# Kernel tuning notes

Measured on AMD Instinct MI355X. Metric: run time of the kernel, lower is better.

Reference implementation:

```python
import jax, jax.numpy as jnp
import numpy as np
from jax import lax

NPOINT = 1024
NSAMPLE = 32
RADIUS = 0.2
EPS = 1e-5  # BatchNorm eps (torch default)


def farthest_point_sample(xyz, npoint):
    # xyz: [B, N, 3] -> [B, npoint] int32 indices. Deterministic start at index 0
    # (torch version uses a random start; math is otherwise identical).
    B, N, _ = xyz.shape

    def step(carry, _):
        distance, farthest = carry
        centroid = jnp.take_along_axis(xyz, farthest[:, None, None], axis=1)  # [B,1,3]
        d = jnp.sum((xyz - centroid) ** 2, axis=-1)                            # [B,N]
        distance = jnp.minimum(distance, d)
        return (distance, jnp.argmax(distance, axis=-1).astype(jnp.int32)), farthest

    init = (jnp.full((B, N), 1e10, xyz.dtype), jnp.zeros((B,), jnp.int32))
    _, cents = lax.scan(step, init, None, length=npoint)  # [npoint, B]
    return cents.T


def query_ball_point(radius, nsample, xyz, new_xyz):
    # xyz: [B,N,3], new_xyz: [B,S,3] -> [B,S,nsample] int32 indices
    B, N, _ = xyz.shape
    S = new_xyz.shape[1]
    sqr = jnp.sum((new_xyz[:, :, None, :] - xyz[:, None, :, :]) ** 2, axis=-1)  # [B,S,N]
    base = jnp.broadcast_to(jnp.arange(N, dtype=jnp.int32), (B, S, N))
    idx = jnp.where(sqr > radius * radius, N, base)
    idx = jnp.sort(idx, axis=-1)[:, :, :nsample]
    first = idx[:, :, :1]
    return jnp.where(idx == N, first, idx)


def index_points(points, idx):
    # points: [B,N,C], idx: [B,...] -> [B,...,C]
    return jax.vmap(lambda p, i: p[i])(points, idx)


def conv_bn_relu(x, w, b, g, beta):
    # 1x1 Conv2d == per-point linear; BatchNorm2d in training mode (batch stats,
    # biased variance) over all dims except channel.
    y = jnp.einsum('bskc,oc->bsko', x, w) + b          # [B,S,K,O]
    m = jnp.mean(y, axis=(0, 1, 2), keepdims=True)
    v = jnp.var(y, axis=(0, 1, 2), keepdims=True)
    return jax.nn.relu((y - m) / jnp.sqrt(v + EPS) * g + beta)


def setup_inputs() -> dict:
    key = jax.random.key(0)
    ks = jax.random.split(key, 8)
    B, N, D = 16, 4096, 64
    xyz = jax.random.uniform(ks[0], (B, N, 3), dtype=jnp.float32)
    points = jax.random.normal(ks[1], (B, N, D), dtype=jnp.float32)
    chans = [D + 3, 64, 64, 128]
    inp = {'xyz': xyz, 'points': points}
    for i in range(3):
        cin, cout = chans[i], chans[i + 1]
        inp[f'w{i}'] = jax.random.normal(ks[2 + i], (cout, cin), dtype=jnp.float32) * (1.0 / np.sqrt(cin))
        inp[f'b{i}'] = jnp.zeros((cout,), jnp.float32)
        inp[f'g{i}'] = jnp.ones((cout,), jnp.float32)
        inp[f'be{i}'] = jnp.zeros((cout,), jnp.float32)
    return inp


def reference(xyz, points, w0, b0, g0, be0, w1, b1, g1, be1, w2, b2, g2, be2):
    fps_idx = farthest_point_sample(xyz, NPOINT)            # [B,S]
    new_xyz = index_points(xyz, fps_idx)                    # [B,S,3]
    group_idx = query_ball_point(RADIUS, NSAMPLE, xyz, new_xyz)  # [B,S,K]
    grouped_xyz = index_points(xyz, group_idx) - new_xyz[:, :, None, :]  # [B,S,K,3]
    feats = jnp.concatenate([grouped_xyz, index_points(points, group_idx)], axis=-1)
    for (w, b, g, be) in ((w0, b0, g0, be0), (w1, b1, g1, be1), (w2, b2, g2, be2)):
        feats = conv_bn_relu(feats, w, b, g, be)
    new_points = jnp.max(feats, axis=2)                     # max over nsample -> [B,S,C_out]
    return new_xyz, new_points
```

## Files before the change

### kernel.cpp

```cpp
#include <hip/hip_runtime.h>
#include <hip/hip_bf16.h>
#include <cstdint>
#include <cstddef>

#define NPTS   4096
#define NPT    1024
#define NSAMP  32
#define NBATCH 16
#define MROWS  (NBATCH*NPT*NSAMP)
#define EPSV   1e-5f

typedef __attribute__((ext_vector_type(8))) short bfrag;
typedef __attribute__((ext_vector_type(4))) float f32x4;
typedef __attribute__((ext_vector_type(2))) float f32x2;

static __device__ __forceinline__ unsigned short f2bf(float f) {
  union { float f; unsigned u; } x; x.f = f;
  unsigned u = x.u;
  u += 0x7FFFu + ((u >> 16) & 1u);
  return (unsigned short)(u >> 16);
}
static __device__ __forceinline__ float bf2f(unsigned short h) {
  union { unsigned u; float f; } x; x.u = ((unsigned)h) << 16;
  return x.f;
}
static __device__ __forceinline__ unsigned cvt_pk_bf16(float lo, float hi) {
  unsigned r;
  asm("v_cvt_pk_bf16_f32 %0, %1, %2" : "=v"(r) : "v"(lo), "v"(hi));
  return r;
}

__global__ __launch_bounds__(256) void prep_kernel(
    const float* __restrict__ w0, const float* __restrict__ w1,
    const float* __restrict__ w2, unsigned short* __restrict__ wb0,
    unsigned short* __restrict__ wb1, unsigned short* __restrict__ wb2) {
  const int tid = threadIdx.x;
  for (int i = tid; i < 64 * 96; i += 256) {
    const int o = i / 96, c = i % 96;
    float v;
    if (c < 64)      v = w0[o * 67 + 3 + c];
    else if (c < 67) v = w0[o * 67 + (c - 64)];
    else             v = 0.f;
    wb0[i] = f2bf(v);
  }
  for (int i = tid; i < 64 * 64; i += 256) wb1[i] = f2bf(w1[i]);
  for (int i = tid; i < 128 * 64; i += 256) wb2[i] = f2bf(w2[i]);
}

#define FPS_T 256
#define PPT   (NPTS / FPS_T)

template <int CTRL>
static __device__ __forceinline__ float dpp_max_step(float v) {
  int t = __builtin_amdgcn_update_dpp(0, __float_as_int(v), CTRL, 0xF, 0xF, true);
  return fmaxf(v, __int_as_float(t));
}

__global__ __launch_bounds__(FPS_T) void fps_kernel(
    const float* __restrict__ xyz, float* __restrict__ out_newxyz) {
  __shared__ __align__(16) float xs[NPTS];
  __shared__ __align__(16) float ys[NPTS];
  __shared__ __align__(16) float zs[NPTS];
  __shared__ __align__(16) float olds[NPT * 3];
  __shared__ __align__(16) uint2 sl[2][4];

  const int b = blockIdx.x;
  const int tid = threadIdx.x;
  const int wave = tid >> 6;
  const float* base = xyz + (size_t)b * NPTS * 3;
  for (int i = tid; i < NPTS; i += FPS_T) {
    xs[i] = base[3 * i + 0];
    ys[i] = base[3 * i + 1];
    zs[i] = base[3 * i + 2];
  }
  __syncthreads();

  const int p0 = tid * PPT;
  f32x2 px2[8], py2[8], pz2[8], d2[8];
  #pragma unroll
  for (int p = 0; p < 8; ++p) {
    px2[p] = f32x2{xs[p0 + 2 * p], xs[p0 + 2 * p + 1]};
    py2[p] = f32x2{ys[p0 + 2 * p], ys[p0 + 2 * p + 1]};
    pz2[p] = f32x2{zs[p0 + 2 * p], zs[p0 + 2 * p + 1]};
    d2[p] = f32x2{1e10f, 1e10f};
  }

  int cur = 0;
  for (int it = 0; it < NPT; ++it) {
    const float cx = xs[cur], cy = ys[cur], cz = zs[cur];
    if (tid == 0) {
      olds[3 * it + 0] = cx;
      olds[3 * it + 1] = cy;
      olds[3 * it + 2] = cz;
    }
    if (it == NPT - 1) break;

    float bestv = -1.f; int besti = p0;
    {
      #pragma clang fp contract(off)
      const f32x2 c2x = {cx, cx}, c2y = {cy, cy}, c2z = {cz, cz};
      #pragma unroll
      for (int p = 0; p < 8; ++p) {
        const f32x2 dx = px2[p] - c2x;
        const f32x2 dy = py2[p] - c2y;
        const f32x2 dz = pz2[p] - c2z;
        const f32x2 s = (dx * dx + dy * dy) + dz * dz;
        f32x2 nd = d2[p];
        nd.x = fminf(nd.x, s.x);
        nd.y = fminf(nd.y, s.y);
        d2[p] = nd;
        const float pmax = fmaxf(nd.x, nd.y);
        const bool yg = nd.y > nd.x;
        const int pidx = p0 + 2 * p + (yg ? 1 : 0);
        const bool g = pmax > bestv;
        bestv = g ? pmax : bestv;
        besti = g ? pidx : besti;
      }
    }

    float m = bestv;
    m = dpp_max_step<0x111>(m);
    m = dpp_max_step<0x112>(m);
    m = dpp_max_step<0x114>(m);
    m = dpp_max_step<0x118>(m);
    m = dpp_max_step<0x142>(m);
    m = dpp_max_step<0x143>(m);
    const float wmax =
        __int_as_float(__builtin_amdgcn_readlane(__float_as_int(m), 63));

    const unsigned long long mask = __ballot(bestv == wmax);
    const int wl = __ffsll((long long)mask) - 1;
    const int widx = __builtin_amdgcn_readlane(besti, wl);

    const int buf = it & 1;
    if ((tid & 63) == 0)
      sl[buf][wave] = make_uint2(__float_as_uint(wmax), (unsigned)widx);
    __syncthreads();

    const uint4* p4 = (const uint4*)&sl[buf][0];
    const uint4 q0 = p4[0], q1 = p4[1];
    float bv; int bi;
    {
      bv = __uint_as_float(q0.x); bi = (int)q0.y;
      const float v1 = __uint_as_float(q0.z);
      if (v1 > bv) { bv = v1; bi = (int)q0.w; }
      const float v2 = __uint_as_float(q1.x);
      if (v2 > bv) { bv = v2; bi = (int)q1.y; }
      const float v3 = __uint_as_float(q1.z);
      if (v3 > bv) { bv = v3; bi = (int)q1.w; }
    }
    cur = bi;
  }

  __syncthreads();
  float* outb = out_newxyz + (size_t)b * NPT * 3;
  for (int i = tid; i < NPT * 3 / 4; i += FPS_T)
    *(float4*)&outb[4 * i] = *(const float4*)&olds[4 * i];
}

__global__ __launch_bounds__(256) void ballquery_kernel(
    const float* __restrict__ xyz, const float* __restrict__ newxyz,
    int* __restrict__ gidx) {
  const int gw = (int)((blockIdx.x * 256 + threadIdx.x) >> 6);
  const int lane = threadIdx.x & 63;
  const int b = gw >> 10, s = gw & 1023;
  const float* base = xyz + (size_t)b * NPTS * 3;
  const float* c = newxyz + (size_t)(b * NPT + s) * 3;
  const float cx = c[0], cy = c[1], cz = c[2];
  const float R2 = (float)(0.2 * 0.2);
  int* g = gidx + (size_t)(b * NPT + s) * NSAMP;

  int count = 0;
  int first = -1;
  for (int ch = 0; ch < NPTS / 64; ++ch) {
    const int i = ch * 64 + lane;
    const float dx = __fsub_rn(base[3 * i + 0], cx);
    const float dy = __fsub_rn(base[3 * i + 1], cy);
    const float dz = __fsub_rn(base[3 * i + 2], cz);
    const float d = __fadd_rn(__fadd_rn(__fmul_rn(dx, dx), __fmul_rn(dy, dy)),
                              __fmul_rn(dz, dz));
    const bool pred = !(d > R2);
    const unsigned long long mask = __ballot(pred);
    if (mask) {
      if (count == 0) first = ch * 64 + (__ffsll((long long)mask) - 1);
      const int rank = __popcll(mask & ((1ull << lane) - 1ull));
      const int pos = count + rank;
      if (pred && pos < NSAMP) g[pos] = i;
      count += (int)__popcll(mask);
      if (count >= NSAMP) break;
    }
  }
  if (first < 0) first = 0;
  for (int j = count + lane; j < NSAMP; j += 64) g[j] = first;
}

__global__ __launch_bounds__(256) void mm1_mfma_kernel(
    const float* __restrict__ xyz, const float* __restrict__ points,
    const float* __restrict__ newxyz, const int* __restrict__ gidx,
    const unsigned short* __restrict__ Wb, unsigned short* __restrict__ Y,
    float* __restrict__ psum, float* __restrict__ psq) {
  constexpr int KP = 104;
  __shared__ __align__(16) unsigned short As[64 * KP];
  __shared__ __align__(16) unsigned short ly[64 * 64];
  __shared__ float ssum[64], ssq[64];
  const int tid = threadIdx.x, bid = blockIdx.x;
  const size_t r0 = (size_t)bid * 64;

  {
    const int row = tid >> 2, q = tid & 3;
    const int gs = bid * 2 + (row >> 5);
    const int b = gs >> 10;
    const int k = row & 31;
    const int gpt = gidx[(size_t)gs * NSAMP + k];
    const float* pf = points + ((size_t)b * NPTS + gpt) * 64 + 16 * q;
    float f[16];
    #pragma unroll
    for (int i = 0; i < 4; ++i)
      *(float4*)&f[4 * i] = *(const float4*)&pf[4 * i];
    uint4 u0, u1;
    u0.x = cvt_pk_bf16(f[0], f[1]);   u0.y = cvt_pk_bf16(f[2], f[3]);
    u0.z = cvt_pk_bf16(f[4], f[5]);   u0.w = cvt_pk_bf16(f[6], f[7]);
    u1.x = cvt_pk_bf16(f[8], f[9]);   u1.y = cvt_pk_bf16(f[10], f[11]);
    u1.z = cvt_pk_bf16(f[12], f[13]); u1.w = cvt_pk_bf16(f[14], f[15]);
    uint4* dst = (uint4*)&As[row * KP + 16 * q];
    dst[0] = u0; dst[1] = u1;
    if (q == 0) {
      const float* px = xyz + ((size_t)b * NPTS + gpt) * 3;
      const float* pc = newxyz + (size_t)gs * 3;
      const float rx = px[0] - pc[0];
      const float ry = px[1] - pc[1];
      const float rz = px[2] - pc[2];
      uint4* d2 = (uint4*)&As[row * KP + 64];
      d2[0] = uint4{cvt_pk_bf16(rx, ry), cvt_pk_bf16(rz, 0.f), 0u, 0u};
      d2[1] = uint4{0u, 0u, 0u, 0u};
      d2[2] = uint4{0u, 0u, 0u, 0u};
      d2[3] = uint4{0u, 0u, 0u, 0u};
    }
  }
  if (tid < 64) { ssum[tid] = 0.f; ssq[tid] = 0.f; }
  __syncthreads();

  const int wave = tid >> 6, lane = tid & 63;
  const int l15 = lane & 15, kq = lane >> 4;
  const unsigned short* abase = &As[(wave * 16 + l15) * KP + kq * 8];
  const bfrag a0 = *(const bfrag*)abase;
  const bfrag a1 = *(const bfrag*)(abase + 32);
  const bfrag a2 = *(const bfrag*)(abase + 64);

  #pragma unroll
  for (int nt = 0; nt < 4; ++nt) {
    const unsigned short* wsrc = Wb + (size_t)(nt * 16 + l15) * 96 + kq * 8;
    const bfrag b0 = *(const bfrag*)wsrc;
    const bfrag b1 = *(const bfrag*)(wsrc + 32);
    const bfrag b2 = *(const bfrag*)(wsrc + 64);
    f32x4 acc = {0.f, 0.f, 0.f, 0.f};
    acc = __builtin_amdgcn_mfma_f32_16x16x32_bf16(a0, b0, acc, 0, 0, 0);
    acc = __builtin_amdgcn_mfma_f32_16x16x32_bf16(a1, b1, acc, 0, 0, 0);
    acc = __builtin_amdgcn_mfma_f32_16x16x32_bf16(a2, b2, acc, 0, 0, 0);

    float s = acc[0] + acc[1] + acc[2] + acc[3];
    float q = acc[0]*acc[0] + acc[1]*acc[1] + acc[2]*acc[2] + acc[3]*acc[3];
    s += __shfl_xor(s, 16); q += __shfl_xor(q, 16);
    s += __shfl_xor(s, 32); q += __shfl_xor(q, 32);
    if (kq == 0) {
      atomicAdd(&ssum[nt * 16 + l15], s);
      atomicAdd(&ssq [nt * 16 + l15], q);
    }
    const unsigned p01 = cvt_pk_bf16(acc[0], acc[1]);
    const unsigned p23 = cvt_pk_bf16(acc[2], acc[3]);
    const int colo = nt * 16 + l15;
    const int rbase = wave * 16 + kq * 4;
    ly[(rbase + 0) * 64 + colo] = (unsigned short)(p01 & 0xffffu);
    ly[(rbase + 1) * 64 + colo] = (unsigned short)(p01 >> 16);
    ly[(rbase + 2) * 64 + colo] = (unsigned short)(p23 & 0xffffu);
    ly[(rbase + 3) * 64 + colo] = (unsigned short)(p23 >> 16);
  }
  __syncthreads();
  {
    const uint4* lsrc = (const uint4*)ly;
    uint4* gdst = (uint4*)(Y + r0 * 64);
    #pragma unroll
    for (int i = tid; i < 64 * 64 * 2 / 16; i += 256) gdst[i] = lsrc[i];
  }
  if (tid < 64) {
    psum[(size_t)bid * 64 + tid] = ssum[tid];
    psq [(size_t)bid * 64 + tid] = ssq [tid];
  }
}

static __device__ __forceinline__ bfrag affine_relu_frag(
    const unsigned short* __restrict__ src, const float* __restrict__ st,
    int c0) {
  union { bfrag f; unsigned u[4]; } r;
  const uint4 raw = *(const uint4*)src;
  const unsigned w[4] = {raw.x, raw.y, raw.z, raw.w};
  #pragma unroll
  for (int p = 0; p < 4; ++p) {
    const int c = c0 + 2 * p;
    float lo = bf2f((unsigned short)(w[p] & 0xffffu));
    float hi = bf2f((unsigned short)(w[p] >> 16));
    lo = fmaxf(fmaf(lo, st[2 * c + 0], st[2 * c + 1]), 0.f);
    hi = fmaxf(fmaf(hi, st[2 * c + 2], st[2 * c + 3]), 0.f);
    r.u[p] = cvt_pk_bf16(lo, hi);
  }
  return r.f;
}

template <int COUT, int WAVES>
__global__ __launch_bounds__(WAVES * 64) void mm_mfma_kernel(
    const unsigned short* __restrict__ Xin, const unsigned short* __restrict__ Wb,
    const float* __restrict__ stin, unsigned short* __restrict__ Y,
    float* __restrict__ psum, float* __restrict__ psq) {
  constexpr int NT = COUT / 16;
  constexpr int ROWS = WAVES * 16;
  __shared__ float ssum[COUT], ssq[COUT];
  __shared__ __align__(16) unsigned short ly[ROWS * COUT];
  const int tid = threadIdx.x, bid = blockIdx.x;
  const int wave = tid >> 6, lane = tid & 63;
  const int l15 = lane & 15, kq = lane >> 4;
  const size_t r0 = (size_t)bid * ROWS;
  if (tid < COUT) { ssum[tid] = 0.f; ssq[tid] = 0.f; }

  const int arow = wave * 16 + l15;
  const unsigned short* asrc = Xin + (r0 + arow) * 64 + kq * 8;
  const bfrag a0 = affine_relu_frag(asrc, stin, kq * 8);
  const bfrag a1 = affine_relu_frag(asrc + 32, stin, 32 + kq * 8);
  __syncthreads();

  #pragma unroll
  for (int nt = 0; nt < NT; ++nt) {
    const unsigned short* wsrc = Wb + (size_t)(nt * 16 + l15) * 64 + kq * 8;
    const bfrag b0 = *(const bfrag*)wsrc;
    const bfrag b1 = *(const bfrag*)(wsrc + 32);
    f32x4 acc = {0.f, 0.f, 0.f, 0.f};
    acc = __builtin_amdgcn_mfma_f32_16x16x32_bf16(a0, b0, acc, 0, 0, 0);
    acc = __builtin_amdgcn_mfma_f32_16x16x32_bf16(a1, b1, acc, 0, 0, 0);

    float s = acc[0] + acc[1] + acc[2] + acc[3];
    float q = acc[0]*acc[0] + acc[1]*acc[1] + acc[2]*acc[2] + acc[3]*acc[3];
    s += __shfl_xor(s, 16); q += __shfl_xor(q, 16);
    s += __shfl_xor(s, 32); q += __shfl_xor(q, 32);
    if (kq == 0) {
      atomicAdd(&ssum[nt * 16 + l15], s);
      atomicAdd(&ssq [nt * 16 + l15], q);
    }
    const unsigned p01 = cvt_pk_bf16(acc[0], acc[1]);
    const unsigned p23 = cvt_pk_bf16(acc[2], acc[3]);
    const int colo = nt * 16 + l15;
    const int rbase = wave * 16 + kq * 4;
    ly[(rbase + 0) * COUT + colo] = (unsigned short)(p01 & 0xffffu);
    ly[(rbase + 1) * COUT + colo] = (unsigned short)(p01 >> 16);
    ly[(rbase + 2) * COUT + colo] = (unsigned short)(p23 & 0xffffu);
    ly[(rbase + 3) * COUT + colo] = (unsigned short)(p23 >> 16);
  }
  __syncthreads();
  {
    const uint4* lsrc = (const uint4*)ly;
    uint4* gdst = (uint4*)(Y + r0 * COUT);
    #pragma unroll
    for (int i = tid; i < ROWS * COUT * 2 / 16; i += WAVES * 64) gdst[i] = lsrc[i];
  }
  if (tid < COUT) {
    psum[(size_t)bid * COUT + tid] = ssum[tid];
    psq [(size_t)bid * COUT + tid] = ssq [tid];
  }
}

__global__ __launch_bounds__(512) void mm3_pool_kernel(
    const unsigned short* __restrict__ Xin, const unsigned short* __restrict__ Wb,
    const float* __restrict__ stin, float* __restrict__ pooled,
    float* __restrict__ psum, float* __restrict__ psq) {
  constexpr int COUT = 128, NT = 8;
  __shared__ float ssum[COUT], ssq[COUT];
  __shared__ float pm[8][COUT];
  const int tid = threadIdx.x, bid = blockIdx.x;
  const int wave = tid >> 6, lane = tid & 63;
  const int l15 = lane & 15, kq = lane >> 4;
  const size_t r0 = (size_t)bid * 128;
  if (tid < COUT) { ssum[tid] = 0.f; ssq[tid] = 0.f; }

  const int arow = wave * 16 + l15;
  const unsigned short* asrc = Xin + (r0 + arow) * 64 + kq * 8;
  const bfrag a0 = affine_relu_frag(asrc, stin, kq * 8);
  const bfrag a1 = affine_relu_frag(asrc + 32, stin, 32 + kq * 8);
  __syncthreads();

  #pragma unroll
  for (int nt = 0; nt < NT; ++nt) {
    const unsigned short* wsrc = Wb + (size_t)(nt * 16 + l15) * 64 + kq * 8;
    const bfrag b0 = *(const bfrag*)wsrc;
    const bfrag b1 = *(const bfrag*)(wsrc + 32);
    f32x4 acc = {0.f, 0.f, 0.f, 0.f};
    acc = __builtin_amdgcn_mfma_f32_16x16x32_bf16(a0, b0, acc, 0, 0, 0);
    acc = __builtin_amdgcn_mfma_f32_16x16x32_bf16(a1, b1, acc, 0, 0, 0);

    float s = acc[0] + acc[1] + acc[2] + acc[3];
    float q = acc[0]*acc[0] + acc[1]*acc[1] + acc[2]*acc[2] + acc[3]*acc[3];
    s += __shfl_xor(s, 16); q += __shfl_xor(q, 16);
    s += __shfl_xor(s, 32); q += __shfl_xor(q, 32);
    float mx = fmaxf(fmaxf(acc[0], acc[1]), fmaxf(acc[2], acc[3]));
    mx = fmaxf(mx, __shfl_xor(mx, 16));
    mx = fmaxf(mx, __shfl_xor(mx, 32));
    if (kq == 0) {
      atomicAdd(&ssum[nt * 16 + l15], s);
      atomicAdd(&ssq [nt * 16 + l15], q);
      pm[wave][nt * 16 + l15] = mx;
    }
  }
  __syncthreads();
  {
    const int g = tid >> 7, col = tid & 127;
    const float v = fmaxf(pm[2 * g][col], pm[2 * g + 1][col]);
    pooled[(r0 >> 5) * COUT + g * COUT + col] = v;
  }
  if (tid < COUT) {
    psum[(size_t)bid * COUT + tid] = ssum[tid];
    psq [(size_t)bid * COUT + tid] = ssq [tid];
  }
}

__global__ __launch_bounds__(256) void finalize_kernel(
    const float* __restrict__ psum, const float* __restrict__ psq,
    const float* __restrict__ gam, const float* __restrict__ bet,
    float* __restrict__ st, int C, int nb) {
  const int c = blockIdx.x, tid = threadIdx.x;
  float s = 0.f, q = 0.f;
  for (int i = tid; i < nb; i += 256) {
    s += psum[(size_t)i * C + c];
    q += psq [(size_t)i * C + c];
  }
  #pragma unroll
  for (int off = 32; off > 0; off >>= 1) {
    s += __shfl_down(s, off);
    q += __shfl_down(q, off);
  }
  __shared__ float as_[4], aq_[4];
  if ((tid & 63) == 0) { as_[tid >> 6] = s; aq_[tid >> 6] = q; }
  __syncthreads();
  if (tid == 0) {
    s = as_[0] + as_[1] + as_[2] + as_[3];
    q = aq_[0] + aq_[1] + aq_[2] + aq_[3];
    const float invM = 1.f / (float)MROWS;
    const float mean = s * invM;
    const float var = q * invM - mean * mean;
    const float inv = 1.f / sqrtf(var + EPSV);
    const float sc = gam[c] * inv;
    st[2 * c + 0] = sc;
    st[2 * c + 1] = bet[c] - mean * sc;
  }
}

__global__ __launch_bounds__(256) void bn_relu_kernel(
    const float* __restrict__ pooled, const float* __restrict__ st,
    float* __restrict__ out) {
  __shared__ float s_st[256];
  const int tid = threadIdx.x;
  s_st[tid] = st[tid];
  __syncthreads();
  const int n4 = NBATCH * NPT * 128 / 4;
  for (int i = blockIdx.x * 256 + tid; i < n4; i += gridDim.x * 256) {
    float4 v = ((const float4*)pooled)[i];
    const int c0 = (i * 4) & 127;
    v.x = fmaxf(fmaf(v.x, s_st[2 * c0 + 0], s_st[2 * c0 + 1]), 0.f);
    v.y = fmaxf(fmaf(v.y, s_st[2 * c0 + 2], s_st[2 * c0 + 3]), 0.f);
    v.z = fmaxf(fmaf(v.z, s_st[2 * c0 + 4], s_st[2 * c0 + 5]), 0.f);
    v.w = fmaxf(fmaf(v.w, s_st[2 * c0 + 6], s_st[2 * c0 + 7]), 0.f);
    ((float4*)out)[i] = v;
  }
}

extern "C" void kernel_launch(void* const* d_in, const int* in_sizes, int n_in,
                              void* d_out, int out_size, void* d_ws, size_t ws_size,
                              hipStream_t stream) {
  (void)in_sizes; (void)n_in; (void)out_size; (void)ws_size;
  const float* xyz    = (const float*)d_in[0];
  const float* points = (const float*)d_in[1];
  const float* w0 = (const float*)d_in[2];
  const float* g0 = (const float*)d_in[4];
  const float* be0 = (const float*)d_in[5];
  const float* w1 = (const float*)d_in[6];
  const float* g1 = (const float*)d_in[8];
  const float* be1 = (const float*)d_in[9];
  const float* w2 = (const float*)d_in[10];
  const float* g2 = (const float*)d_in[12];
  const float* be2 = (const float*)d_in[13];

  float* out = (float*)d_out;
  float* newxyz = out;
  float* newpts = out + (size_t)NBATCH * NPT * 3;

  char* ws = (char*)d_ws;
  unsigned short* Y1 = (unsigned short*)ws;
  float* P3 = (float*)ws;
  unsigned short* Y2 = (unsigned short*)(ws + 134217728);
  int*   gidx = (int*)  (ws + 201326592);
  float* psum = (float*)(ws + 203423744);
  float* psq  = (float*)(ws + 205520896);
  float* st   = (float*)(ws + 207618048);
  float* st1 = st, *st2 = st + 256, *st3 = st + 512;
  unsigned short* wb0 = (unsigned short*)(ws + 207621120);
  unsigned short* wb1 = (unsigned short*)(ws + 207621120 + 12288);
  unsigned short* wb2 = (unsigned short*)(ws + 207621120 + 12288 + 8192);

  prep_kernel<<<1, 256, 0, stream>>>(w0, w1, w2, wb0, wb1, wb2);
  fps_kernel<<<NBATCH, FPS_T, 0, stream>>>(xyz, newxyz);
  ballquery_kernel<<<(NBATCH * NPT) / 4, 256, 0, stream>>>(xyz, newxyz, gidx);
  mm1_mfma_kernel<<<MROWS / 64, 256, 0, stream>>>(xyz, points, newxyz, gidx, wb0, Y1, psum, psq);
  finalize_kernel<<<64, 256, 0, stream>>>(psum, psq, g0, be0, st1, 64, MROWS / 64);
  mm_mfma_kernel<64, 4><<<MROWS / 64, 256, 0, stream>>>(Y1, wb1, st1, Y2, psum, psq);
  finalize_kernel<<<64, 256, 0, stream>>>(psum, psq, g1, be1, st2, 64, MROWS / 64);
  mm3_pool_kernel<<<MROWS / 128, 512, 0, stream>>>(Y2, wb2, st2, P3, psum, psq);
  finalize_kernel<<<128, 256, 0, stream>>>(psum, psq, g2, be2, st3, 128, MROWS / 128);
  bn_relu_kernel<<<2048, 256, 0, stream>>>(P3, st3, newpts);
}
```

Measured before the change: 863.4 us.

## Fuse FPS, ball query and first matmul into one persistent producer-consumer kernel

Merges the farthest-point-sampling, ball-query and first MFMA layer into a single persistent kernel. Sixteen blocks run FPS and publish centroids in chunks of 128 through global progress counters. The remaining blocks pull tiles from an atomic work counter, spin-wait until their centroids are ready, then run the ball query into shared memory and the first matmul. The point is to overlap the long serial FPS with downstream work and to drop the global group-index buffer. The cost is spin-waiting on flags, a dependence on all blocks being co-resident, and an FPS loop that is no longer vectorised as float2.

```diff
diff --git a/kernel.cpp b/kernel.cpp
--- a/kernel.cpp
+++ b/kernel.cpp
@@ -8,11 +8,11 @@
 #define NSAMP  32
 #define NBATCH 16
 #define MROWS  (NBATCH*NPT*NSAMP)
+#define NTILES (MROWS / 64)
 #define EPSV   1e-5f
 
 typedef __attribute__((ext_vector_type(8))) short bfrag;
 typedef __attribute__((ext_vector_type(4))) float f32x4;
-typedef __attribute__((ext_vector_type(2))) float f32x2;
 
 static __device__ __forceinline__ unsigned short f2bf(float f) {
   union { float f; unsigned u; } x; x.f = f;
@@ -33,8 +33,10 @@
 __global__ __launch_bounds__(256) void prep_kernel(
     const float* __restrict__ w0, const float* __restrict__ w1,
     const float* __restrict__ w2, unsigned short* __restrict__ wb0,
-    unsigned short* __restrict__ wb1, unsigned short* __restrict__ wb2) {
+    unsigned short* __restrict__ wb1, unsigned short* __restrict__ wb2,
+    int* __restrict__ flags) {
   const int tid = threadIdx.x;
+  for (int i = tid; i < 260; i += 256) flags[i] = 0;
   for (int i = tid; i < 64 * 96; i += 256) {
     const int o = i / 96, c = i % 96;
     float v;
@@ -49,6 +51,7 @@
 
 #define FPS_T 256
 #define PPT   (NPTS / FPS_T)
+#define CHUNK 128
 
 template <int CTRL>
 static __device__ __forceinline__ float dpp_max_step(float v) {
@@ -56,235 +59,255 @@
   return fmaxf(v, __int_as_float(t));
 }
 
-__global__ __launch_bounds__(FPS_T) void fps_kernel(
-    const float* __restrict__ xyz, float* __restrict__ out_newxyz) {
+__global__ __launch_bounds__(256) void k1_kernel(
+    const float* __restrict__ xyz, const float* __restrict__ points,
+    const unsigned short* __restrict__ Wb, float* __restrict__ newxyz,
+    unsigned short* __restrict__ Y1, float* __restrict__ psum,
+    float* __restrict__ psq, int* __restrict__ flags) {
   __shared__ __align__(16) float xs[NPTS];
   __shared__ __align__(16) float ys[NPTS];
   __shared__ __align__(16) float zs[NPTS];
   __shared__ __align__(16) float olds[NPT * 3];
   __shared__ __align__(16) uint2 sl[2][4];
-
-  const int b = blockIdx.x;
-  const int tid = threadIdx.x;
-  const int wave = tid >> 6;
-  const float* base = xyz + (size_t)b * NPTS * 3;
-  for (int i = tid; i < NPTS; i += FPS_T) {
-    xs[i] = base[3 * i + 0];
-    ys[i] = base[3 * i + 1];
-    zs[i] = base[3 * i + 2];
-  }
-  __syncthreads();
-
-  const int p0 = tid * PPT;
-  f32x2 px2[8], py2[8], pz2[8], d2[8];
-  #pragma unroll
-  for (int p = 0; p < 8; ++p) {
-    px2[p] = f32x2{xs[p0 + 2 * p], xs[p0 + 2 * p + 1]};
-    py2[p] = f32x2{ys[p0 + 2 * p], ys[p0 + 2 * p + 1]};
-    pz2[p] = f32x2{zs[p0 + 2 * p], zs[p0 + 2 * p + 1]};
-    d2[p] = f32x2{1e10f, 1e10f};
-  }
-
-  int cur = 0;
-  for (int it = 0; it < NPT; ++it) {
-    const float cx = xs[cur], cy = ys[cur], cz = zs[cur];
-    if (tid == 0) {
-      olds[3 * it + 0] = cx;
-      olds[3 * it + 1] = cy;
-      olds[3 * it + 2] = cz;
-    }
-    if (it == NPT - 1) break;
-
-    float bestv = -1.f; int besti = p0;
-    {
-      #pragma clang fp contract(off)
-      const f32x2 c2x = {cx, cx}, c2y = {cy, cy}, c2z = {cz, cz};
-      #pragma unroll
-      for (int p = 0; p < 8; ++p) {
-        const f32x2 dx = px2[p] - c2x;
-        const f32x2 dy = py2[p] - c2y;
-        const f32x2 dz = pz2[p] - c2z;
-        const f32x2 s = (dx * dx + dy * dy) + dz * dz;
-        f32x2 nd = d2[p];
-        nd.x = fminf(nd.x, s.x);
-        nd.y = fminf(nd.y, s.y);
-        d2[p] = nd;
-        const float pmax = fmaxf(nd.x, nd.y);
-        const bool yg = nd.y > nd.x;
-        const int pidx = p0 + 2 * p + (yg ? 1 : 0);
-        const bool g = pmax > bestv;
-        bestv = g ? pmax : bestv;
-        besti = g ? pidx : besti;
-      }
-    }
-
-    float m = bestv;
-    m = dpp_max_step<0x111>(m);
-    m = dpp_max_step<0x112>(m);
-    m = dpp_max_step<0x114>(m);
-    m = dpp_max_step<0x118>(m);
-    m = dpp_max_step<0x142>(m);
-    m = dpp_max_step<0x143>(m);
-    const float wmax =
-        __int_as_float(__builtin_amdgcn_readlane(__float_as_int(m), 63));
-
-    const unsigned long long mask = __ballot(bestv == wmax);
-    const int wl = __ffsll((long long)mask) - 1;
-    const int widx = __builtin_amdgcn_readlane(besti, wl);
-
-    const int buf = it & 1;
-    if ((tid & 63) == 0)
-      sl[buf][wave] = make_uint2(__float_as_uint(wmax), (unsigned)widx);
-    __syncthreads();
-
-    const uint4* p4 = (const uint4*)&sl[buf][0];
-    const uint4 q0 = p4[0], q1 = p4[1];
-    float bv; int bi;
-    {
-      bv = __uint_as_float(q0.x); bi = (int)q0.y;
-      const float v1 = __uint_as_float(q0.z);
-      if (v1 > bv) { bv = v1; bi = (int)q0.w; }
-      const float v2 = __uint_as_float(q1.x);
-      if (v2 > bv) { bv = v2; bi = (int)q1.y; }
-      const float v3 = __uint_as_float(q1.z);
-      if (v3 > bv) { bv = v3; bi = (int)q1.w; }
-    }
-    cur = bi;
-  }
-
-  __syncthreads();
-  float* outb = out_newxyz + (size_t)b * NPT * 3;
-  for (int i = tid; i < NPT * 3 / 4; i += FPS_T)
-    *(float4*)&outb[4 * i] = *(const float4*)&olds[4 * i];
-}
-
-__global__ __launch_bounds__(256) void ballquery_kernel(
-    const float* __restrict__ xyz, const float* __restrict__ newxyz,
-    int* __restrict__ gidx) {
-  const int gw = (int)((blockIdx.x * 256 + threadIdx.x) >> 6);
-  const int lane = threadIdx.x & 63;
-  const int b = gw >> 10, s = gw & 1023;
-  const float* base = xyz + (size_t)b * NPTS * 3;
-  const float* c = newxyz + (size_t)(b * NPT + s) * 3;
-  const float cx = c[0], cy = c[1], cz = c[2];
-  const float R2 = (float)(0.2 * 0.2);
-  int* g = gidx + (size_t)(b * NPT + s) * NSAMP;
-
-  int count = 0;
-  int first = -1;
-  for (int ch = 0; ch < NPTS / 64; ++ch) {
-    const int i = ch * 64 + lane;
-    const float dx = __fsub_rn(base[3 * i + 0], cx);
-    const float dy = __fsub_rn(base[3 * i + 1], cy);
-    const float dz = __fsub_rn(base[3 * i + 2], cz);
-    const float d = __fadd_rn(__fadd_rn(__fmul_rn(dx, dx), __fmul_rn(dy, dy)),
-                              __fmul_rn(dz, dz));
-    const bool pred = !(d > R2);
-    const unsigned long long mask = __ballot(pred);
-    if (mask) {
-      if (count == 0) first = ch * 64 + (__ffsll((long long)mask) - 1);
-      const int rank = __popcll(mask & ((1ull << lane) - 1ull));
-      const int pos = count + rank;
-      if (pred && pos < NSAMP) g[pos] = i;
-      count += (int)__popcll(mask);
-      if (count >= NSAMP) break;
-    }
-  }
-  if (first < 0) first = 0;
-  for (int j = count + lane; j < NSAMP; j += 64) g[j] = first;
-}
-
-__global__ __launch_bounds__(256) void mm1_mfma_kernel(
-    const float* __restrict__ xyz, const float* __restrict__ points,
-    const float* __restrict__ newxyz, const int* __restrict__ gidx,
-    const unsigned short* __restrict__ Wb, unsigned short* __restrict__ Y,
-    float* __restrict__ psum, float* __restrict__ psq) {
   constexpr int KP = 104;
   __shared__ __align__(16) unsigned short As[64 * KP];
   __shared__ __align__(16) unsigned short ly[64 * 64];
   __shared__ float ssum[64], ssq[64];
-  const int tid = threadIdx.x, bid = blockIdx.x;
-  const size_t r0 = (size_t)bid * 64;
-
-  {
-    const int row = tid >> 2, q = tid & 3;
-    const int gs = bid * 2 + (row >> 5);
-    const int b = gs >> 10;
-    const int k = row & 31;
-    const int gpt = gidx[(size_t)gs * NSAMP + k];
-    const float* pf = points + ((size_t)b * NPTS + gpt) * 64 + 16 * q;
-    float f[16];
+  __shared__ int   gidxL[64];
+  __shared__ float cents[8];
+  __shared__ int   s_tile;
+
+  const int tid = threadIdx.x;
+  int* progress = flags;
+  int* counter  = flags + 256;
+
+  if (blockIdx.x < NBATCH) {
+    const int b = blockIdx.x;
+    const int wave = tid >> 6;
+    const float* base = xyz + (size_t)b * NPTS * 3;
+    float* outb = newxyz + (size_t)b * NPT * 3;
+    int* prog = &progress[b * 16];
+    for (int i = tid; i < NPTS; i += FPS_T) {
+      xs[i] = base[3 * i + 0];
+      ys[i] = base[3 * i + 1];
+      zs[i] = base[3 * i + 2];
+    }
+    __syncthreads();
+
+    const int p0 = tid * PPT;
+    float px[PPT], py[PPT], pz[PPT], dist[PPT];
     #pragma unroll
-    for (int i = 0; i < 4; ++i)
-      *(float4*)&f[4 * i] = *(const float4*)&pf[4 * i];
-    uint4 u0, u1;
-    u0.x = cvt_pk_bf16(f[0], f[1]);   u0.y = cvt_pk_bf16(f[2], f[3]);
-    u0.z = cvt_pk_bf16(f[4], f[5]);   u0.w = cvt_pk_bf16(f[6], f[7]);
-    u1.x = cvt_pk_bf16(f[8], f[9]);   u1.y = cvt_pk_bf16(f[10], f[11]);
-    u1.z = cvt_pk_bf16(f[12], f[13]); u1.w = cvt_pk_bf16(f[14], f[15]);
-    uint4* dst = (uint4*)&As[row * KP + 16 * q];
-    dst[0] = u0; dst[1] = u1;
-    if (q == 0) {
-      const float* px = xyz + ((size_t)b * NPTS + gpt) * 3;
-      const float* pc = newxyz + (size_t)gs * 3;
-      const float rx = px[0] - pc[0];
-      const float ry = px[1] - pc[1];
-      const float rz = px[2] - pc[2];
-      uint4* d2 = (uint4*)&As[row * KP + 64];
-      d2[0] = uint4{cvt_pk_bf16(rx, ry), cvt_pk_bf16(rz, 0.f), 0u, 0u};
-      d2[1] = uint4{0u, 0u, 0u, 0u};
-      d2[2] = uint4{0u, 0u, 0u, 0u};
-      d2[3] = uint4{0u, 0u, 0u, 0u};
-    }
-  }
-  if (tid < 64) { ssum[tid] = 0.f; ssq[tid] = 0.f; }
-  __syncthreads();
+    for (int i = 0; i < PPT; i += 4) {
+      *(float4*)&px[i] = *(const float4*)&xs[p0 + i];
+      *(float4*)&py[i] = *(const float4*)&ys[p0 + i];
+      *(float4*)&pz[i] = *(const float4*)&zs[p0 + i];
+    }
+    #pragma unroll
+    for (int i = 0; i < PPT; ++i) dist[i] = 1e10f;
+
+    int cur = 0;
+    for (int it = 0; it < NPT; ++it) {
+      const float cx = xs[cur], cy = ys[cur], cz = zs[cur];
+      if (tid == 0) {
+        olds[3 * it + 0] = cx;
+        olds[3 * it + 1] = cy;
+        olds[3 * it + 2] = cz;
+      }
+      if ((it & (CHUNK - 1)) == CHUNK - 1) {
+        __syncthreads();
+        const int cs = it - (CHUNK - 1);
+        if (tid < 96)
+          *(float4*)&outb[cs * 3 + tid * 4] =
+              *(const float4*)&olds[cs * 3 + tid * 4];
+        __threadfence();
+        __syncthreads();
+        if (tid == 0) atomicAdd(prog, CHUNK);
+      }
+      if (it == NPT - 1) break;
+
+      float bestv = -1.f; int besti = p0;
+      #pragma unroll
+      for (int i = 0; i < PPT; ++i) {
+        const float dx = __fsub_rn(px[i], cx);
+        const float dy = __fsub_rn(py[i], cy);
+        const float dz = __fsub_rn(pz[i], cz);
+        const float d = __fadd_rn(__fadd_rn(__fmul_rn(dx, dx), __fmul_rn(dy, dy)),
+                                  __fmul_rn(dz, dz));
+        const float nd = fminf(dist[i], d);
+        dist[i] = nd;
+        const bool g = nd > bestv;
+        bestv = g ? nd : bestv;
+        besti = g ? (p0 + i) : besti;
+      }
+
+      float m = bestv;
+      m = dpp_max_step<0x111>(m);
+      m = dpp_max_step<0x112>(m);
+      m = dpp_max_step<0x114>(m);
+      m = dpp_max_step<0x118>(m);
+      m = dpp_max_step<0x142>(m);
+      m = dpp_max_step<0x143>(m);
+      const float wmax =
+          __int_as_float(__builtin_amdgcn_readlane(__float_as_int(m), 63));
+
+      const unsigned long long mask = __ballot(bestv == wmax);
+      const int wl = __ffsll((long long)mask) - 1;
+      const int widx = __builtin_amdgcn_readlane(besti, wl);
+
+      const int buf = it & 1;
+      if ((tid & 63) == 0)
+        sl[buf][wave] = make_uint2(__float_as_uint(wmax), (unsigned)widx);
+      __syncthreads();
+
+      const uint4* p4 = (const uint4*)&sl[buf][0];
+      const uint4 q0 = p4[0], q1 = p4[1];
+      float bv; int bi;
+      {
+        bv = __uint_as_float(q0.x); bi = (int)q0.y;
+        const float v1 = __uint_as_float(q0.z);
+        if (v1 > bv) { bv = v1; bi = (int)q0.w; }
+        const float v2 = __uint_as_float(q1.x);
+        if (v2 > bv) { bv = v2; bi = (int)q1.y; }
+        const float v3 = __uint_as_float(q1.z);
+        if (v3 > bv) { bv = v3; bi = (int)q1.w; }
+      }
+      cur = bi;
+    }
+    return;
+  }
 
   const int wave = tid >> 6, lane = tid & 63;
-  const int l15 = lane & 15, kq = lane >> 4;
-  const unsigned short* abase = &As[(wave * 16 + l15) * KP + kq * 8];
-  const bfrag a0 = *(const bfrag*)abase;
-  const bfrag a1 = *(const bfrag*)(abase + 32);
-  const bfrag a2 = *(const bfrag*)(abase + 64);
-
-  #pragma unroll
-  for (int nt = 0; nt < 4; ++nt) {
-    const unsigned short* wsrc = Wb + (size_t)(nt * 16 + l15) * 96 + kq * 8;
-    const bfrag b0 = *(const bfrag*)wsrc;
-    const bfrag b1 = *(const bfrag*)(wsrc + 32);
-    const bfrag b2 = *(const bfrag*)(wsrc + 64);
-    f32x4 acc = {0.f, 0.f, 0.f, 0.f};
-    acc = __builtin_amdgcn_mfma_f32_16x16x32_bf16(a0, b0, acc, 0, 0, 0);
-    acc = __builtin_amdgcn_mfma_f32_16x16x32_bf16(a1, b1, acc, 0, 0, 0);
-    acc = __builtin_amdgcn_mfma_f32_16x16x32_bf16(a2, b2, acc, 0, 0, 0);
-
-    float s = acc[0] + acc[1] + acc[2] + acc[3];
-    float q = acc[0]*acc[0] + acc[1]*acc[1] + acc[2]*acc[2] + acc[3]*acc[3];
-    s += __shfl_xor(s, 16); q += __shfl_xor(q, 16);
-    s += __shfl_xor(s, 32); q += __shfl_xor(q, 32);
-    if (kq == 0) {
-      atomicAdd(&ssum[nt * 16 + l15], s);
-      atomicAdd(&ssq [nt * 16 + l15], q);
-    }
-    const unsigned p01 = cvt_pk_bf16(acc[0], acc[1]);
-    const unsigned p23 = cvt_pk_bf16(acc[2], acc[3]);
-    const int colo = nt * 16 + l15;
-    const int rbase = wave * 16 + kq * 4;
-    ly[(rbase + 0) * 64 + colo] = (unsigned short)(p01 & 0xffffu);
-    ly[(rbase + 1) * 64 + colo] = (unsigned short)(p01 >> 16);
-    ly[(rbase + 2) * 64 + colo] = (unsigned short)(p23 & 0xffffu);
-    ly[(rbase + 3) * 64 + colo] = (unsigned short)(p23 >> 16);
-  }
-  __syncthreads();
-  {
-    const uint4* lsrc = (const uint4*)ly;
-    uint4* gdst = (uint4*)(Y + r0 * 64);
+  for (;;) {
+    if (tid == 0) {
+      const int t0 = atomicAdd(counter, 1);
+      s_tile = t0;
+      if (t0 < NTILES) {
+        const int b = t0 & 15, s0 = (t0 >> 4) * 2;
+        while (__hip_atomic_load(&progress[b * 16], __ATOMIC_ACQUIRE,
+                                 __HIP_MEMORY_SCOPE_AGENT) < s0 + 2)
+          __builtin_amdgcn_s_sleep(2);
+      }
+    }
+    __syncthreads();
+    const int t = s_tile;
+    if (t >= NTILES) break;
+    const int b = t & 15, s0 = (t >> 4) * 2;
+
+    if (wave < 2) {
+      const int gs = b * NPT + s0 + wave;
+      const float* base = xyz + (size_t)b * NPTS * 3;
+      const float* c = newxyz + (size_t)gs * 3;
+      const float cx = c[0], cy = c[1], cz = c[2];
+      if (lane == 0) {
+        cents[wave * 4 + 0] = cx;
+        cents[wave * 4 + 1] = cy;
+        cents[wave * 4 + 2] = cz;
+      }
+      const float R2 = (float)(0.2 * 0.2);
+      int* g = &gidxL[wave * 32];
+      int count = 0;
+      int first = -1;
+      for (int ch = 0; ch < NPTS / 64; ++ch) {
+        const int i = ch * 64 + lane;
+        const float dx = __fsub_rn(base[3 * i + 0], cx);
+        const float dy = __fsub_rn(base[3 * i + 1], cy);
+        const float dz = __fsub_rn(base[3 * i + 2], cz);
+        const float d = __fadd_rn(
+            __fadd_rn(__fmul_rn(dx, dx), __fmul_rn(dy, dy)), __fmul_rn(dz, dz));
+        const bool pred = !(d > R2);
+        const unsigned long long mask = __ballot(pred);
+        if (mask) {
+          if (count == 0) first = ch * 64 + (__ffsll((long long)mask) - 1);
+          const int rank = __popcll(mask & ((1ull << lane) - 1ull));
+          const int pos = count + rank;
+          if (pred && pos < NSAMP) g[pos] = i;
+          count += (int)__popcll(mask);
+          if (count >= NSAMP) break;
+        }
+      }
+      if (first < 0) first = 0;
+      for (int j = count + lane; j < NSAMP; j += 64) g[j] = first;
+    }
+    if (tid < 64) { ssum[tid] = 0.f; ssq[tid] = 0.f; }
+    __syncthreads();
+
+    {
+      const int row = tid >> 2, q = tid & 3;
+      const int gpt = gidxL[row];
+      const float* pf = points + ((size_t)b * NPTS + gpt) * 64 + 16 * q;
+      float f[16];
+      #pragma unroll
+      for (int i = 0; i < 4; ++i)
+        *(float4*)&f[4 * i] = *(const float4*)&pf[4 * i];
+      uint4 u0, u1;
+      u0.x = cvt_pk_bf16(f[0], f[1]);   u0.y = cvt_pk_bf16(f[2], f[3]);
+      u0.z = cvt_pk_bf16(f[4], f[5]);   u0.w = cvt_pk_bf16(f[6], f[7]);
+      u1.x = cvt_pk_bf16(f[8], f[9]);   u1.y = cvt_pk_bf16(f[10], f[11]);
+      u1.z = cvt_pk_bf16(f[12], f[13]); u1.w = cvt_pk_bf16(f[14], f[15]);
+      uint4* dst = (uint4*)&As[row * KP + 16 * q];
+      dst[0] = u0; dst[1] = u1;
+      if (q == 0) {
+        const float* px = xyz + ((size_t)b * NPTS + gpt) * 3;
+        const float* pc = &cents[(row >> 5) * 4];
+        const float rx = px[0] - pc[0];
+        const float ry = px[1] - pc[1];
+        const float rz = px[2] - pc[2];
+        uint4* d2 = (uint4*)&As[row * KP + 64];
+        d2[0] = uint4{cvt_pk_bf16(rx, ry), cvt_pk_bf16(rz, 0.f), 0u, 0u};
+        d2[1] = uint4{0u, 0u, 0u, 0u};
+        d2[2] = uint4{0u, 0u, 0u, 0u};
+        d2[3] = uint4{0u, 0u, 0u, 0u};
+      }
+    }
+    __syncthreads();
+
+    const int l15 = lane & 15, kq = lane >> 4;
+    const unsigned short* abase = &As[(wave * 16 + l15) * KP + kq * 8];
+    const bfrag a0 = *(const bfrag*)abase;
+    const bfrag a1 = *(const bfrag*)(abase + 32);
+    const bfrag a2 = *(const bfrag*)(abase + 64);
+
     #pragma unroll
-    for (int i = tid; i < 64 * 64 * 2 / 16; i += 256) gdst[i] = lsrc[i];
-  }
-  if (tid < 64) {
-    psum[(size_t)bid * 64 + tid] = ssum[tid];
-    psq [(size_t)bid * 64 + tid] = ssq [tid];
+    for (int nt = 0; nt < 4; ++nt) {
+      const unsigned short* wsrc = Wb + (size_t)(nt * 16 + l15) * 96 + kq * 8;
+      const bfrag b0 = *(const bfrag*)wsrc;
+      const bfrag b1 = *(const bfrag*)(wsrc + 32);
+      const bfrag b2 = *(const bfrag*)(wsrc + 64);
+      f32x4 acc = {0.f, 0.f, 0.f, 0.f};
+      acc = __builtin_amdgcn_mfma_f32_16x16x32_bf16(a0, b0, acc, 0, 0, 0);
+      acc = __builtin_amdgcn_mfma_f32_16x16x32_bf16(a1, b1, acc, 0, 0, 0);
+      acc = __builtin_amdgcn_mfma_f32_16x16x32_bf16(a2, b2, acc, 0, 0, 0);
+
+      float s = acc[0] + acc[1] + acc[2] + acc[3];
+      float q = acc[0]*acc[0] + acc[1]*acc[1] + acc[2]*acc[2] + acc[3]*acc[3];
+      s += __shfl_xor(s, 16); q += __shfl_xor(q, 16);
+      s += __shfl_xor(s, 32); q += __shfl_xor(q, 32);
+      if (kq == 0) {
+        atomicAdd(&ssum[nt * 16 + l15], s);
+        atomicAdd(&ssq [nt * 16 + l15], q);
+      }
+      const unsigned p01 = cvt_pk_bf16(acc[0], acc[1]);
+      const unsigned p23 = cvt_pk_bf16(acc[2], acc[3]);
+      const int colo = nt * 16 + l15;
+      const int rbase = wave * 16 + kq * 4;
+      ly[(rbase + 0) * 64 + colo] = (unsigned short)(p01 & 0xffffu);
+      ly[(rbase + 1) * 64 + colo] = (unsigned short)(p01 >> 16);
+      ly[(rbase + 2) * 64 + colo] = (unsigned short)(p23 & 0xffffu);
+      ly[(rbase + 3) * 64 + colo] = (unsigned short)(p23 >> 16);
+    }
+    __syncthreads();
+    {
+      const size_t r0 = (size_t)b * 32768 + (size_t)(t >> 4) * 64;
+      const uint4* lsrc = (const uint4*)ly;
+      uint4* gdst = (uint4*)(Y1 + r0 * 64);
+      #pragma unroll
+      for (int i = tid; i < 64 * 64 * 2 / 16; i += 256) gdst[i] = lsrc[i];
+    }
+    if (tid < 64) {
+      psum[(size_t)t * 64 + tid] = ssum[tid];
+      psq [(size_t)t * 64 + tid] = ssq [tid];
+    }
+    __syncthreads();
   }
 }
 
@@ -493,7 +516,7 @@
   unsigned short* Y1 = (unsigned short*)ws;
   float* P3 = (float*)ws;
   unsigned short* Y2 = (unsigned short*)(ws + 134217728);
-  int*   gidx = (int*)  (ws + 201326592);
+  int*   flags = (int*)(ws + 201326592);
   float* psum = (float*)(ws + 203423744);
   float* psq  = (float*)(ws + 205520896);
   float* st   = (float*)(ws + 207618048);
@@ -502,11 +525,9 @@
   unsigned short* wb1 = (unsigned short*)(ws + 207621120 + 12288);
   unsigned short* wb2 = (unsigned short*)(ws + 207621120 + 12288 + 8192);
 
-  prep_kernel<<<1, 256, 0, stream>>>(w0, w1, w2, wb0, wb1, wb2);
-  fps_kernel<<<NBATCH, FPS_T, 0, stream>>>(xyz, newxyz);
-  ballquery_kernel<<<(NBATCH * NPT) / 4, 256, 0, stream>>>(xyz, newxyz, gidx);
-  mm1_mfma_kernel<<<MROWS / 64, 256, 0, stream>>>(xyz, points, newxyz, gidx, wb0, Y1, psum, psq);
-  finalize_kernel<<<64, 256, 0, stream>>>(psum, psq, g0, be0, st1, 64, MROWS / 64);
+  prep_kernel<<<1, 256, 0, stream>>>(w0, w1, w2, wb0, wb1, wb2, flags);
+  k1_kernel<<<256, 256, 0, stream>>>(xyz, points, wb0, newxyz, Y1, psum, psq, flags);
+  finalize_kernel<<<64, 256, 0, stream>>>(psum, psq, g0, be0, st1, 64, NTILES);
   mm_mfma_kernel<64, 4><<<MROWS / 64, 256, 0, stream>>>(Y1, wb1, st1, Y2, psum, psq);
   finalize_kernel<<<64, 256, 0, stream>>>(psum, psq, g1, be1, st2, 64, MROWS / 64);
   mm3_pool_kernel<<<MROWS / 128, 512, 0, stream>>>(Y2, wb2, st2, P3, psum, psq);
```

Result: slower. 902.1 us (+4.5%).
